# Kernel optimization log

Measured on AMD Instinct MI355X. Metric: run time of the kernel, lower is better.

The kernel has to match this reference:

```python
import jax, jax.numpy as jnp
import numpy as np

B, N, K, NB = 8, 4096, 16, 8
MAX_RADIUS = 10.0
OUT_MUL = 64  # irreps_out = '64x1o' -> output dim 64*3 = 192


def setup_inputs() -> dict:
    key = jax.random.key(0)
    k1, k2 = jax.random.split(key)
    coords = jax.random.normal(k1, (B, N, 3), dtype=jnp.float32)
    tp_weight = jax.random.normal(k2, (1, NB, OUT_MUL), dtype=jnp.float32)
    return {"coords": coords, "tp_weight": tp_weight}


def _knn_indices(coords, k):
    # coords: [B, N, 3] -> nbr idx [B, N, k] (no self loops), per-batch kNN
    n = coords.shape[1]
    d2 = jnp.sum((coords[:, :, None, :] - coords[:, None, :, :]) ** 2, axis=-1)  # [B,N,N]
    d2 = jnp.where(jnp.eye(n, dtype=bool)[None], jnp.inf, d2)
    _, idx = jax.lax.top_k(-d2, k)  # k nearest
    return idx


def reference(coords, tp_weight):
    nbr = _knn_indices(coords, K)                                # [B,N,K] int32
    nbr_coords = jax.vmap(lambda c, i: c[i])(coords, nbr)        # [B,N,K,3]
    r = nbr_coords - coords[:, :, None, :]                       # sender - receiver
    dist = jnp.linalg.norm(r, axis=-1, keepdims=True)            # [B,N,K,1]
    rhat = r / (dist + 1e-8)                                     # 1x1o input
    cutoff = jnp.clip(dist / MAX_RADIUS, 0.0, 1.0)
    # gaussian soft one-hot over [0,1] with NB centers
    centers = jnp.linspace(0.0, 1.0, NB, dtype=coords.dtype)
    sigma = 1.0 / NB
    g = jnp.exp(-((cutoff - centers) ** 2) / (2.0 * sigma * sigma))  # [B,N,K,NB]
    s = jnp.sum(g, axis=-1, keepdims=True)
    rb = g / jnp.where(s > 0, s, jnp.ones_like(s))               # 8x0e input
    # FullyConnectedTensorProduct 1x1o x NBx0e -> OUT_MULx1o (shared weights)
    # path normalization: 1/sqrt(mul_in1 * mul_in2) = 1/sqrt(NB)
    alpha = 1.0 / np.sqrt(1 * NB)
    W = tp_weight[0]                                             # [NB, OUT_MUL]
    edge_feat = alpha * jnp.einsum('vw,bnkv,bnkm->bnkwm', W, rb, rhat)  # [B,N,K,64,3]
    # exactly k incoming edges per receiver -> scatter_mean == mean over K
    agg = jnp.mean(edge_feat, axis=2).reshape(B, N, OUT_MUL * 3)  # [B,N,192]
    return agg
```

## Files before the change

kernel.cpp:

```cpp
#include <hip/hip_runtime.h>

typedef unsigned int u32;
typedef unsigned long long u64;
typedef float v2f __attribute__((ext_vector_type(2)));

#define NBATCH 8
#define NPTS   4096
#define NQTOT  (NBATCH * NPTS)
#define KNN    16
#define NBASIS 8
#define OUTM   64
#define NSPLIT 8
#define WIN    (NPTS / NSPLIT)
#define QPB    64
#define TKNN   (QPB * NSPLIT)
#define GRP    8
#define BUFCAP 64
#define ROWSTR 81
#define TOFF   64

#define SENT 0x7f800000ffffffffull

__device__ __forceinline__ void ce(u64& x, u64& y) {
  u64 a = x, b = y;
  bool sw = b < a;
  x = sw ? b : a;
  y = sw ? a : b;
}

template <int N>
__device__ __forceinline__ void oems_sort(u64* a) {
#pragma unroll
  for (int p = 1; p < N; p <<= 1) {
#pragma unroll
    for (int k = p; k >= 1; k >>= 1) {
#pragma unroll
      for (int j = k & (p - 1); j + k < N; j += 2 * k) {
#pragma unroll
        for (int i = 0; i < k; ++i) {
          int lo = i + j, hi = i + j + k;
          if (hi < N && (lo / (2 * p)) == (hi / (2 * p)))
            ce(a[lo], a[hi]);
        }
      }
    }
  }
}

__device__ __forceinline__ void merge16(u64 t[16], const u64 a[16]) {
  u64 m[16];
#pragma unroll
  for (int i = 0; i < 16; ++i) {
    u64 x = t[i], y = a[15 - i];
    m[i] = (x < y) ? x : y;
  }
#pragma unroll
  for (int k = 8; k >= 1; k >>= 1) {
#pragma unroll
    for (int i = 0; i < 16; ++i) {
      if ((i & k) == 0) ce(m[i], m[i | k]);
    }
  }
#pragma unroll
  for (int i = 0; i < 16; ++i) t[i] = m[i];
}

__device__ __forceinline__ v2f d2pair(v2f cx, v2f cy, v2f cz, v2f qx, v2f qy,
                                      v2f qz) {
#pragma clang fp contract(off)
  v2f dx = cx - qx;
  v2f dy = cy - qy;
  v2f dz = cz - qz;
  v2f d2 = (dx * dx + dy * dy) + dz * dz;
  return d2;
}

__global__ __launch_bounds__(TKNN) void se3_kernel(
    const float* __restrict__ Xp, const float* __restrict__ Yp,
    const float* __restrict__ Zp, const float4* __restrict__ cpad,
    const float* __restrict__ Wmat, float* __restrict__ out) {
  __shared__ u64 sBuf[QPB * ROWSTR];
  __shared__ u32 sCnt[QPB];
  __shared__ float sThr[QPB];
  __shared__ float sM[QPB * 25];

  const int b = blockIdx.x;
  const int qg = blockIdx.y;
  const int tid = threadIdx.x;
  const int ql = tid & 63;
  const int sp = tid >> 6;
  const int qi = qg * QPB + ql;
  const int base = b * NPTS;

  if (tid < QPB) sCnt[tid] = 0;

  const float qx = Xp[base + qi];
  const float qy = Yp[base + qi];
  const float qz = Zp[base + qi];
  const v2f qxx = {qx, qx}, qyy = {qy, qy}, qzz = {qz, qz};

  const int wbase = __builtin_amdgcn_readfirstlane(sp * WIN);
  const v2f* xs2 = (const v2f*)(Xp + base + wbase);
  const v2f* ys2 = (const v2f*)(Yp + base + wbase);
  const v2f* zs2 = (const v2f*)(Zp + base + wbase);
  const int sj = qi - wbase;

  {
    u64 s16[16];
    float cd[16];
#pragma unroll
    for (int p = 0; p < 8; ++p) {
      v2f d2 = d2pair(xs2[p], ys2[p], zs2[p], qxx, qyy, qzz);
      cd[2 * p + 0] = d2.x;
      cd[2 * p + 1] = d2.y;
    }
#pragma unroll
    for (int i = 0; i < 16; ++i) {
      u64 v = ((u64)__float_as_uint(cd[i]) << 32) | (u32)(wbase + i);
      s16[i] = (i == sj) ? SENT : v;
    }
    oems_sort<16>(s16);

    if (sp >= 1 && sp <= 4) {
#pragma unroll
      for (int e = 0; e < 16; ++e)
        sBuf[ql * ROWSTR + (sp - 1) * 16 + e] = s16[e];
    }
    __syncthreads();
    if (sp == 0) {
      u64 t16[16];
#pragma unroll
      for (int e = 0; e < 16; ++e) t16[e] = s16[e];
#pragma unroll
      for (int s = 0; s < 4; ++s) {
        u64 a[16];
#pragma unroll
        for (int e = 0; e < 16; ++e) a[e] = sBuf[ql * ROWSTR + s * 16 + e];
        merge16(t16, a);
      }
#pragma unroll
      for (int e = 0; e < 16; ++e) sBuf[ql * ROWSTR + TOFF + e] = t16[e];
    }
    __syncthreads();
    if (sp >= 5) {
#pragma unroll
      for (int e = 0; e < 16; ++e)
        sBuf[ql * ROWSTR + (sp - 5) * 16 + e] = s16[e];
    }
    __syncthreads();
    if (sp == 0) {
      u64 t16[16];
#pragma unroll
      for (int e = 0; e < 16; ++e) t16[e] = sBuf[ql * ROWSTR + TOFF + e];
#pragma unroll
      for (int s = 0; s < 3; ++s) {
        u64 a[16];
#pragma unroll
        for (int e = 0; e < 16; ++e) a[e] = sBuf[ql * ROWSTR + s * 16 + e];
        merge16(t16, a);
      }
#pragma unroll
      for (int e = 0; e < 16; ++e) sBuf[ql * ROWSTR + TOFF + e] = t16[e];
      sThr[ql] = __uint_as_float((u32)(t16[15] >> 32));
    }
    __syncthreads();
  }
  float thr = sThr[ql];

  const int selfgrp = (sj >= 0 && sj < WIN) ? (sj >> 3) : -1;
  const u32 selfbit = 1u << (sj & 7);

#pragma unroll
  for (int ph = 0; ph < 5; ++ph) {
    const int cstart = 16 << ph;
    const int cend = 32 << ph;
    for (int g = cstart; g < cend; g += GRP) {
      v2f d2p[4];
#pragma unroll
      for (int p = 0; p < 4; ++p)
        d2p[p] = d2pair(xs2[(g >> 1) + p], ys2[(g >> 1) + p],
                        zs2[(g >> 1) + p], qxx, qyy, qzz);
      u32 want = 0;
#pragma unroll
      for (int i = 0; i < GRP; ++i)
        want |= (d2p[i >> 1][i & 1] <= thr) ? (1u << i) : 0u;
      if ((g >> 3) == selfgrp) want &= ~selfbit;
      if (__any(want)) {
#pragma unroll
        for (int i = 0; i < GRP; ++i) {
          if (want & (1u << i)) {
            u32 slot = atomicAdd(&sCnt[ql], 1u);
            if (slot < BUFCAP)
              sBuf[ql * ROWSTR + slot] =
                  ((u64)__float_as_uint(d2p[i >> 1][i & 1]) << 32) |
                  (u32)(wbase + g + i);
          }
        }
      }
    }
    __syncthreads();
    if (sp == ph + 1) {
      int n = (int)sCnt[ql];
      n = n < BUFCAP ? n : BUFCAP;
      if (__any(n > 0)) {
        u64 t16[16];
#pragma unroll
        for (int e = 0; e < 16; ++e) t16[e] = sBuf[ql * ROWSTR + TOFF + e];
        for (int k = 0; __any(k < n); k += 16) {
          u64 a[16];
#pragma unroll
          for (int e = 0; e < 16; ++e)
            a[e] = (k + e < n) ? sBuf[ql * ROWSTR + k + e] : SENT;
          oems_sort<16>(a);
          merge16(t16, a);
        }
#pragma unroll
        for (int e = 0; e < 16; ++e) sBuf[ql * ROWSTR + TOFF + e] = t16[e];
        sThr[ql] = __uint_as_float((u32)(t16[15] >> 32));
      }
      sCnt[ql] = 0;
    }
    __syncthreads();
    thr = sThr[ql];
  }

  if (sp < 4) {
    const int k = sp;
    u64 pv[4];
#pragma unroll
    for (int e = 0; e < 4; ++e)
      pv[e] = sBuf[ql * ROWSTR + TOFF + k * 4 + e];
    float4 nc[4];
    float dd[4];
#pragma unroll
    for (int e = 0; e < 4; ++e) {
      nc[e] = cpad[base + (int)(u32)pv[e]];
      dd[e] = __uint_as_float((u32)(pv[e] >> 32));
    }
    float M[24];
#pragma unroll
    for (int j = 0; j < 24; ++j) M[j] = 0.f;
#pragma unroll
    for (int e = 0; e < 4; ++e) {
      float rx = nc[e].x - qx;
      float ry = nc[e].y - qy;
      float rz = nc[e].z - qz;
      float dist = sqrtf(dd[e]);
      float inv = 1.0f / (dist + 1e-8f);
      rx *= inv; ry *= inv; rz *= inv;
      float cut = fminf(dist * 0.1f, 1.0f);
      float g[NBASIS], s = 0.f;
#pragma unroll
      for (int v = 0; v < NBASIS; ++v) {
        float t = cut - (float)v * (1.0f / 7.0f);
        g[v] = __expf(-32.0f * t * t);
        s += g[v];
      }
      float rs = 1.0f / s;
#pragma unroll
      for (int v = 0; v < NBASIS; ++v) {
        float rb = g[v] * rs;
        M[v * 3 + 0] = fmaf(rb, rx, M[v * 3 + 0]);
        M[v * 3 + 1] = fmaf(rb, ry, M[v * 3 + 1]);
        M[v * 3 + 2] = fmaf(rb, rz, M[v * 3 + 2]);
      }
    }
    float* fp = (float*)(sBuf + ql * ROWSTR);
#pragma unroll
    for (int c = 0; c < 24; ++c) fp[k * 25 + c] = M[c];
  }
  __syncthreads();

  {
    const float* fp = (const float*)(sBuf + ql * ROWSTR);
#pragma unroll
    for (int j0 = 0; j0 < 3; ++j0) {
      int j = sp * 3 + j0;
      float s = fp[0 * 25 + j] + fp[1 * 25 + j] + fp[2 * 25 + j] +
                fp[3 * 25 + j];
      sM[ql * 25 + j] = s;
    }
  }
  __syncthreads();

  float wreg[NBASIS];
#pragma unroll
  for (int v = 0; v < NBASIS; ++v) wreg[v] = Wmat[v * OUTM + ql];
  const float scale = 0.022097086912079608f;
#pragma unroll
  for (int i = 0; i < 8; ++i) {
    int q = sp * 8 + i;
    const float* mq = sM + q * 25;
    float a0 = 0.f, a1 = 0.f, a2 = 0.f;
#pragma unroll
    for (int v = 0; v < NBASIS; ++v) {
      a0 = fmaf(wreg[v], mq[v * 3 + 0], a0);
      a1 = fmaf(wreg[v], mq[v * 3 + 1], a1);
      a2 = fmaf(wreg[v], mq[v * 3 + 2], a2);
    }
    size_t o = (size_t)(base + qg * QPB + q) * (OUTM * 3) + ql * 3;
    out[o + 0] = a0 * scale;
    out[o + 1] = a1 * scale;
    out[o + 2] = a2 * scale;
  }
}

__global__ void prep_kernel(const float* __restrict__ coords,
                            float* __restrict__ Xp, float* __restrict__ Yp,
                            float* __restrict__ Zp, float4* __restrict__ cpad) {
  int i = blockIdx.x * 256 + threadIdx.x;
  if (i < NQTOT) {
    float x = coords[3 * i + 0];
    float y = coords[3 * i + 1];
    float z = coords[3 * i + 2];
    Xp[i] = x; Yp[i] = y; Zp[i] = z;
    cpad[i] = make_float4(x, y, z, 0.f);
  }
}

extern "C" void kernel_launch(void* const* d_in, const int* in_sizes, int n_in,
                              void* d_out, int out_size, void* d_ws, size_t ws_size,
                              hipStream_t stream) {
  const float* coords = (const float*)d_in[0];
  const float* Wmat = (const float*)d_in[1];
  float* out = (float*)d_out;

  char* w = (char*)d_ws;
  float* Xp = (float*)(w);
  float* Yp = (float*)(w + 131072);
  float* Zp = (float*)(w + 262144);
  float4* cpad = (float4*)(w + 393216);

  prep_kernel<<<dim3((NQTOT + 255) / 256), dim3(256), 0, stream>>>(coords, Xp, Yp, Zp, cpad);
  se3_kernel<<<dim3(NBATCH, NPTS / QPB), dim3(TKNN), 0, stream>>>(Xp, Yp, Zp, cpad, Wmat, out);
}
```

Measured before the change: 180.0 us.

## Screen kNN candidates with expanded-norm dot-product test and exact recheck

Replaces the per-candidate squared-distance computation in the candidate scan with an expanded form, 0.5*|c|^2 - c·q, compared against a per-query adjusted threshold. The half-norms are precomputed in the prep kernel and the scan uses 4-wide FMA chains with a group-level min as an early reject. Exact distances are recomputed only for candidates that pass, so the stored keys and ordering stay identical. This lowers ALU work per candidate, with a small safety margin to absorb rounding differences. The float4 padded coordinate array is dropped and the final stage gathers neighbours from the SoA arrays instead.

```diff
diff --git a/kernel.cpp b/kernel.cpp
--- a/kernel.cpp
+++ b/kernel.cpp
@@ -3,6 +3,7 @@
 typedef unsigned int u32;
 typedef unsigned long long u64;
 typedef float v2f __attribute__((ext_vector_type(2)));
+typedef float v4f __attribute__((ext_vector_type(4)));
 
 #define NBATCH 8
 #define NPTS   4096
@@ -18,6 +19,7 @@
 #define BUFCAP 64
 #define ROWSTR 81
 #define TOFF   64
+#define PMARGIN 2e-3f
 
 #define SENT 0x7f800000ffffffffull
 
@@ -75,9 +77,18 @@
   return d2;
 }
 
+__device__ __forceinline__ float d2s(float cx, float cy, float cz, float qx,
+                                     float qy, float qz) {
+#pragma clang fp contract(off)
+  float dx = cx - qx;
+  float dy = cy - qy;
+  float dz = cz - qz;
+  return (dx * dx + dy * dy) + dz * dz;
+}
+
 __global__ __launch_bounds__(TKNN) void se3_kernel(
     const float* __restrict__ Xp, const float* __restrict__ Yp,
-    const float* __restrict__ Zp, const float4* __restrict__ cpad,
+    const float* __restrict__ Zp, const float* __restrict__ Hp,
     const float* __restrict__ Wmat, float* __restrict__ out) {
   __shared__ u64 sBuf[QPB * ROWSTR];
   __shared__ u32 sCnt[QPB];
@@ -98,11 +109,18 @@
   const float qy = Yp[base + qi];
   const float qz = Zp[base + qi];
   const v2f qxx = {qx, qx}, qyy = {qy, qy}, qzz = {qz, qz};
+  const v4f qx4 = {qx, qx, qx, qx};
+  const v4f qy4 = {qy, qy, qy, qy};
+  const v4f qz4 = {qz, qz, qz, qz};
 
   const int wbase = __builtin_amdgcn_readfirstlane(sp * WIN);
   const v2f* xs2 = (const v2f*)(Xp + base + wbase);
   const v2f* ys2 = (const v2f*)(Yp + base + wbase);
   const v2f* zs2 = (const v2f*)(Zp + base + wbase);
+  const v4f* x4 = (const v4f*)(Xp + base + wbase);
+  const v4f* y4 = (const v4f*)(Yp + base + wbase);
+  const v4f* z4 = (const v4f*)(Zp + base + wbase);
+  const v4f* h4 = (const v4f*)(Hp + base + wbase);
   const int sj = qi - wbase;
 
   {
@@ -167,6 +185,9 @@
   }
   float thr = sThr[ql];
 
+  const float qn = qx * qx + qy * qy + qz * qz;
+  float sthr = 0.5f * (thr + PMARGIN - qn);
+
   const int selfgrp = (sj >= 0 && sj < WIN) ? (sj >> 3) : -1;
   const u32 selfbit = 1u << (sj & 7);
 
@@ -175,25 +196,43 @@
     const int cstart = 16 << ph;
     const int cend = 32 << ph;
     for (int g = cstart; g < cend; g += GRP) {
-      v2f d2p[4];
-#pragma unroll
-      for (int p = 0; p < 4; ++p)
-        d2p[p] = d2pair(xs2[(g >> 1) + p], ys2[(g >> 1) + p],
-                        zs2[(g >> 1) + p], qxx, qyy, qzz);
-      u32 want = 0;
-#pragma unroll
-      for (int i = 0; i < GRP; ++i)
-        want |= (d2p[i >> 1][i & 1] <= thr) ? (1u << i) : 0u;
-      if ((g >> 3) == selfgrp) want &= ~selfbit;
-      if (__any(want)) {
-#pragma unroll
-        for (int i = 0; i < GRP; ++i) {
-          if (want & (1u << i)) {
-            u32 slot = atomicAdd(&sCnt[ql], 1u);
-            if (slot < BUFCAP)
-              sBuf[ql * ROWSTR + slot] =
-                  ((u64)__float_as_uint(d2p[i >> 1][i & 1]) << 32) |
-                  (u32)(wbase + g + i);
+      const int gq = g >> 2;
+      v4f XA = x4[gq], XB = x4[gq + 1];
+      v4f YA = y4[gq], YB = y4[gq + 1];
+      v4f ZA = z4[gq], ZB = z4[gq + 1];
+      v4f HA = h4[gq], HB = h4[gq + 1];
+      v4f sA = __builtin_elementwise_fma(
+          -ZA, qz4,
+          __builtin_elementwise_fma(
+              -YA, qy4, __builtin_elementwise_fma(-XA, qx4, HA)));
+      v4f sB = __builtin_elementwise_fma(
+          -ZB, qz4,
+          __builtin_elementwise_fma(
+              -YB, qy4, __builtin_elementwise_fma(-XB, qx4, HB)));
+      v4f m4 = __builtin_elementwise_min(sA, sB);
+      float m = fminf(fminf(m4.x, m4.y), fminf(m4.z, m4.w));
+      if (__any(m <= sthr)) {
+        u32 want = 0;
+#pragma unroll
+        for (int i = 0; i < 4; ++i)
+          want |= (sA[i] <= sthr) ? (1u << i) : 0u;
+#pragma unroll
+        for (int i = 0; i < 4; ++i)
+          want |= (sB[i] <= sthr) ? (1u << (4 + i)) : 0u;
+        if ((g >> 3) == selfgrp) want &= ~selfbit;
+        if (__any(want)) {
+#pragma unroll
+          for (int i = 0; i < GRP; ++i) {
+            if (want & (1u << i)) {
+              float cx = (i < 4) ? XA[i & 3] : XB[i & 3];
+              float cy = (i < 4) ? YA[i & 3] : YB[i & 3];
+              float cz = (i < 4) ? ZA[i & 3] : ZB[i & 3];
+              float d2 = d2s(cx, cy, cz, qx, qy, qz);
+              u32 slot = atomicAdd(&sCnt[ql], 1u);
+              if (slot < BUFCAP)
+                sBuf[ql * ROWSTR + slot] =
+                    ((u64)__float_as_uint(d2) << 32) | (u32)(wbase + g + i);
+            }
           }
         }
       }
@@ -222,6 +261,7 @@
     }
     __syncthreads();
     thr = sThr[ql];
+    sthr = 0.5f * (thr + PMARGIN - qn);
   }
 
   if (sp < 4) {
@@ -230,11 +270,14 @@
 #pragma unroll
     for (int e = 0; e < 4; ++e)
       pv[e] = sBuf[ql * ROWSTR + TOFF + k * 4 + e];
-    float4 nc[4];
+    float ncx[4], ncy[4], ncz[4];
     float dd[4];
 #pragma unroll
     for (int e = 0; e < 4; ++e) {
-      nc[e] = cpad[base + (int)(u32)pv[e]];
+      int id = base + (int)(u32)pv[e];
+      ncx[e] = Xp[id];
+      ncy[e] = Yp[id];
+      ncz[e] = Zp[id];
       dd[e] = __uint_as_float((u32)(pv[e] >> 32));
     }
     float M[24];
@@ -242,9 +285,9 @@
     for (int j = 0; j < 24; ++j) M[j] = 0.f;
 #pragma unroll
     for (int e = 0; e < 4; ++e) {
-      float rx = nc[e].x - qx;
-      float ry = nc[e].y - qy;
-      float rz = nc[e].z - qz;
+      float rx = ncx[e] - qx;
+      float ry = ncy[e] - qy;
+      float rz = ncz[e] - qz;
       float dist = sqrtf(dd[e]);
       float inv = 1.0f / (dist + 1e-8f);
       rx *= inv; ry *= inv; rz *= inv;
@@ -307,14 +350,14 @@
 
 __global__ void prep_kernel(const float* __restrict__ coords,
                             float* __restrict__ Xp, float* __restrict__ Yp,
-                            float* __restrict__ Zp, float4* __restrict__ cpad) {
+                            float* __restrict__ Zp, float* __restrict__ Hp) {
   int i = blockIdx.x * 256 + threadIdx.x;
   if (i < NQTOT) {
     float x = coords[3 * i + 0];
     float y = coords[3 * i + 1];
     float z = coords[3 * i + 2];
     Xp[i] = x; Yp[i] = y; Zp[i] = z;
-    cpad[i] = make_float4(x, y, z, 0.f);
+    Hp[i] = 0.5f * (x * x + y * y + z * z);
   }
 }
 
@@ -329,8 +372,8 @@
   float* Xp = (float*)(w);
   float* Yp = (float*)(w + 131072);
   float* Zp = (float*)(w + 262144);
-  float4* cpad = (float4*)(w + 393216);
-
-  prep_kernel<<<dim3((NQTOT + 255) / 256), dim3(256), 0, stream>>>(coords, Xp, Yp, Zp, cpad);
-  se3_kernel<<<dim3(NBATCH, NPTS / QPB), dim3(TKNN), 0, stream>>>(Xp, Yp, Zp, cpad, Wmat, out);
-}
+  float* Hp = (float*)(w + 393216);
+
+  prep_kernel<<<dim3((NQTOT + 255) / 256), dim3(256), 0, stream>>>(coords, Xp, Yp, Zp, Hp);
+  se3_kernel<<<dim3(NBATCH, NPTS / QPB), dim3(TKNN), 0, stream>>>(Xp, Yp, Zp, Hp, Wmat, out);
+}
```

Result: slower. 184.2 us (+2.3%).

## Split each query's candidate scan across 16 windows with tree-merged top-k

Applied to the files above, without the earlier changes.

Doubles the number of window splits per query, so each block now has 1024 threads that each scan a 256-point window. The serial merge on split 0 is replaced by a pairwise tree reduction of the sorted 16-element lists through shared memory. The threshold-filter phases drop from 5 to 4, and the output loop is spread over twice as many threads. The aim is more parallelism and a shorter serial merge chain, at the cost of more barriers, larger blocks and higher register pressure under the 1024-thread launch bound.

```diff
diff --git a/kernel.cpp b/kernel.cpp
--- a/kernel.cpp
+++ b/kernel.cpp
@@ -10,7 +10,7 @@
 #define KNN    16
 #define NBASIS 8
 #define OUTM   64
-#define NSPLIT 8
+#define NSPLIT 16
 #define WIN    (NPTS / NSPLIT)
 #define QPB    64
 #define TKNN   (QPB * NSPLIT)
@@ -75,6 +75,18 @@
   return d2;
 }
 
+__device__ __forceinline__ void pub16(u64* row, int seg, const u64 s[16]) {
+#pragma unroll
+  for (int e = 0; e < 16; ++e) row[seg * 16 + e] = s[e];
+}
+
+__device__ __forceinline__ void mrg16(const u64* row, int seg, u64 s[16]) {
+  u64 a[16];
+#pragma unroll
+  for (int e = 0; e < 16; ++e) a[e] = row[seg * 16 + e];
+  merge16(s, a);
+}
+
 __global__ __launch_bounds__(TKNN) void se3_kernel(
     const float* __restrict__ Xp, const float* __restrict__ Yp,
     const float* __restrict__ Zp, const float4* __restrict__ cpad,
@@ -105,6 +117,8 @@
   const v2f* zs2 = (const v2f*)(Zp + base + wbase);
   const int sj = qi - wbase;
 
+  u64* row = sBuf + ql * ROWSTR;
+
   {
     u64 s16[16];
     float cd[16];
@@ -121,47 +135,29 @@
     }
     oems_sort<16>(s16);
 
-    if (sp >= 1 && sp <= 4) {
-#pragma unroll
-      for (int e = 0; e < 16; ++e)
-        sBuf[ql * ROWSTR + (sp - 1) * 16 + e] = s16[e];
-    }
+    if (sp >= 8 && sp < 12) pub16(row, sp - 8, s16);
+    __syncthreads();
+    if (sp < 4) mrg16(row, sp, s16);
+    __syncthreads();
+    if (sp >= 12) pub16(row, sp - 12, s16);
+    __syncthreads();
+    if (sp >= 4 && sp < 8) mrg16(row, sp - 4, s16);
+    __syncthreads();
+    if (sp >= 4 && sp < 8) pub16(row, sp - 4, s16);
+    __syncthreads();
+    if (sp < 4) mrg16(row, sp, s16);
+    __syncthreads();
+    if (sp == 2 || sp == 3) pub16(row, sp - 2, s16);
+    __syncthreads();
+    if (sp < 2) mrg16(row, sp, s16);
+    __syncthreads();
+    if (sp == 1) pub16(row, 0, s16);
     __syncthreads();
     if (sp == 0) {
-      u64 t16[16];
-#pragma unroll
-      for (int e = 0; e < 16; ++e) t16[e] = s16[e];
-#pragma unroll
-      for (int s = 0; s < 4; ++s) {
-        u64 a[16];
-#pragma unroll
-        for (int e = 0; e < 16; ++e) a[e] = sBuf[ql * ROWSTR + s * 16 + e];
-        merge16(t16, a);
-      }
-#pragma unroll
-      for (int e = 0; e < 16; ++e) sBuf[ql * ROWSTR + TOFF + e] = t16[e];
-    }
-    __syncthreads();
-    if (sp >= 5) {
-#pragma unroll
-      for (int e = 0; e < 16; ++e)
-        sBuf[ql * ROWSTR + (sp - 5) * 16 + e] = s16[e];
-    }
-    __syncthreads();
-    if (sp == 0) {
-      u64 t16[16];
-#pragma unroll
-      for (int e = 0; e < 16; ++e) t16[e] = sBuf[ql * ROWSTR + TOFF + e];
-#pragma unroll
-      for (int s = 0; s < 3; ++s) {
-        u64 a[16];
-#pragma unroll
-        for (int e = 0; e < 16; ++e) a[e] = sBuf[ql * ROWSTR + s * 16 + e];
-        merge16(t16, a);
-      }
-#pragma unroll
-      for (int e = 0; e < 16; ++e) sBuf[ql * ROWSTR + TOFF + e] = t16[e];
-      sThr[ql] = __uint_as_float((u32)(t16[15] >> 32));
+      mrg16(row, 0, s16);
+#pragma unroll
+      for (int e = 0; e < 16; ++e) row[TOFF + e] = s16[e];
+      sThr[ql] = __uint_as_float((u32)(s16[15] >> 32));
     }
     __syncthreads();
   }
@@ -171,7 +167,7 @@
   const u32 selfbit = 1u << (sj & 7);
 
 #pragma unroll
-  for (int ph = 0; ph < 5; ++ph) {
+  for (int ph = 0; ph < 4; ++ph) {
     const int cstart = 16 << ph;
     const int cend = 32 << ph;
     for (int g = cstart; g < cend; g += GRP) {
@@ -205,17 +201,17 @@
       if (__any(n > 0)) {
         u64 t16[16];
 #pragma unroll
-        for (int e = 0; e < 16; ++e) t16[e] = sBuf[ql * ROWSTR + TOFF + e];
+        for (int e = 0; e < 16; ++e) t16[e] = row[TOFF + e];
         for (int k = 0; __any(k < n); k += 16) {
           u64 a[16];
 #pragma unroll
           for (int e = 0; e < 16; ++e)
-            a[e] = (k + e < n) ? sBuf[ql * ROWSTR + k + e] : SENT;
+            a[e] = (k + e < n) ? row[k + e] : SENT;
           oems_sort<16>(a);
           merge16(t16, a);
         }
 #pragma unroll
-        for (int e = 0; e < 16; ++e) sBuf[ql * ROWSTR + TOFF + e] = t16[e];
+        for (int e = 0; e < 16; ++e) row[TOFF + e] = t16[e];
         sThr[ql] = __uint_as_float((u32)(t16[15] >> 32));
       }
       sCnt[ql] = 0;
@@ -229,7 +225,7 @@
     u64 pv[4];
 #pragma unroll
     for (int e = 0; e < 4; ++e)
-      pv[e] = sBuf[ql * ROWSTR + TOFF + k * 4 + e];
+      pv[e] = row[TOFF + k * 4 + e];
     float4 nc[4];
     float dd[4];
 #pragma unroll
@@ -265,14 +261,14 @@
         M[v * 3 + 2] = fmaf(rb, rz, M[v * 3 + 2]);
       }
     }
-    float* fp = (float*)(sBuf + ql * ROWSTR);
+    float* fp = (float*)row;
 #pragma unroll
     for (int c = 0; c < 24; ++c) fp[k * 25 + c] = M[c];
   }
   __syncthreads();
 
-  {
-    const float* fp = (const float*)(sBuf + ql * ROWSTR);
+  if (sp < 8) {
+    const float* fp = (const float*)row;
 #pragma unroll
     for (int j0 = 0; j0 < 3; ++j0) {
       int j = sp * 3 + j0;
@@ -288,8 +284,8 @@
   for (int v = 0; v < NBASIS; ++v) wreg[v] = Wmat[v * OUTM + ql];
   const float scale = 0.022097086912079608f;
 #pragma unroll
-  for (int i = 0; i < 8; ++i) {
-    int q = sp * 8 + i;
+  for (int i = 0; i < 4; ++i) {
+    int q = sp * 4 + i;
     const float* mq = sM + q * 25;
     float a0 = 0.f, a1 = 0.f, a2 = 0.f;
 #pragma unroll
```

Measured after the change: 190.4 us. 5.8% more time.

## Buffer kNN candidates as group bitmasks and recompute distances at merge time

Applied to the files above, without the earlier changes.

During the candidate scan, each thread now does one shared atomic per group of 8 points that has any hits and stores a packed (mask, base index) word, replacing one atomic and one 64-bit store per candidate. The merging thread unpacks these bitmasks, gathers neighbour coordinates from global memory and recomputes the distances before sorting and merging. This moves atomic contention and LDS traffic off the hot scan loop, but adds global gathers and serial bit extraction to the merge step. Because the buffer now holds up to 64 groups rather than 64 candidates, overflow is much less likely. The scan loop is also unrolled by two.

```diff
diff --git a/kernel.cpp b/kernel.cpp
--- a/kernel.cpp
+++ b/kernel.cpp
@@ -15,7 +15,7 @@
 #define QPB    64
 #define TKNN   (QPB * NSPLIT)
 #define GRP    8
-#define BUFCAP 64
+#define ECAP   64
 #define ROWSTR 81
 #define TOFF   64
 
@@ -75,6 +75,15 @@
   return d2;
 }
 
+__device__ __forceinline__ float d2s(float cx, float cy, float cz, float qx,
+                                     float qy, float qz) {
+#pragma clang fp contract(off)
+  float dx = cx - qx;
+  float dy = cy - qy;
+  float dz = cz - qz;
+  return (dx * dx + dy * dy) + dz * dz;
+}
+
 __global__ __launch_bounds__(TKNN) void se3_kernel(
     const float* __restrict__ Xp, const float* __restrict__ Yp,
     const float* __restrict__ Zp, const float4* __restrict__ cpad,
@@ -105,6 +114,8 @@
   const v2f* zs2 = (const v2f*)(Zp + base + wbase);
   const int sj = qi - wbase;
 
+  u64* row = sBuf + (size_t)ql * ROWSTR;
+
   {
     u64 s16[16];
     float cd[16];
@@ -123,8 +134,7 @@
 
     if (sp >= 1 && sp <= 4) {
 #pragma unroll
-      for (int e = 0; e < 16; ++e)
-        sBuf[ql * ROWSTR + (sp - 1) * 16 + e] = s16[e];
+      for (int e = 0; e < 16; ++e) row[(sp - 1) * 16 + e] = s16[e];
     }
     __syncthreads();
     if (sp == 0) {
@@ -135,32 +145,31 @@
       for (int s = 0; s < 4; ++s) {
         u64 a[16];
 #pragma unroll
-        for (int e = 0; e < 16; ++e) a[e] = sBuf[ql * ROWSTR + s * 16 + e];
+        for (int e = 0; e < 16; ++e) a[e] = row[s * 16 + e];
         merge16(t16, a);
       }
 #pragma unroll
-      for (int e = 0; e < 16; ++e) sBuf[ql * ROWSTR + TOFF + e] = t16[e];
+      for (int e = 0; e < 16; ++e) row[TOFF + e] = t16[e];
     }
     __syncthreads();
     if (sp >= 5) {
 #pragma unroll
-      for (int e = 0; e < 16; ++e)
-        sBuf[ql * ROWSTR + (sp - 5) * 16 + e] = s16[e];
+      for (int e = 0; e < 16; ++e) row[(sp - 5) * 16 + e] = s16[e];
     }
     __syncthreads();
     if (sp == 0) {
       u64 t16[16];
 #pragma unroll
-      for (int e = 0; e < 16; ++e) t16[e] = sBuf[ql * ROWSTR + TOFF + e];
+      for (int e = 0; e < 16; ++e) t16[e] = row[TOFF + e];
 #pragma unroll
       for (int s = 0; s < 3; ++s) {
         u64 a[16];
 #pragma unroll
-        for (int e = 0; e < 16; ++e) a[e] = sBuf[ql * ROWSTR + s * 16 + e];
+        for (int e = 0; e < 16; ++e) a[e] = row[s * 16 + e];
         merge16(t16, a);
       }
 #pragma unroll
-      for (int e = 0; e < 16; ++e) sBuf[ql * ROWSTR + TOFF + e] = t16[e];
+      for (int e = 0; e < 16; ++e) row[TOFF + e] = t16[e];
       sThr[ql] = __uint_as_float((u32)(t16[15] >> 32));
     }
     __syncthreads();
@@ -169,11 +178,14 @@
 
   const int selfgrp = (sj >= 0 && sj < WIN) ? (sj >> 3) : -1;
   const u32 selfbit = 1u << (sj & 7);
+
+  u32* ebuf = (u32*)row;
 
 #pragma unroll
   for (int ph = 0; ph < 5; ++ph) {
     const int cstart = 16 << ph;
     const int cend = 32 << ph;
+#pragma unroll 2
     for (int g = cstart; g < cend; g += GRP) {
       v2f d2p[4];
 #pragma unroll
@@ -185,37 +197,53 @@
       for (int i = 0; i < GRP; ++i)
         want |= (d2p[i >> 1][i & 1] <= thr) ? (1u << i) : 0u;
       if ((g >> 3) == selfgrp) want &= ~selfbit;
-      if (__any(want)) {
-#pragma unroll
-        for (int i = 0; i < GRP; ++i) {
-          if (want & (1u << i)) {
-            u32 slot = atomicAdd(&sCnt[ql], 1u);
-            if (slot < BUFCAP)
-              sBuf[ql * ROWSTR + slot] =
-                  ((u64)__float_as_uint(d2p[i >> 1][i & 1]) << 32) |
-                  (u32)(wbase + g + i);
-          }
-        }
+      if (want) {
+        u32 slot = atomicAdd(&sCnt[ql], 1u);
+        if (slot < ECAP) ebuf[slot] = (want << 12) | (u32)(wbase + g);
       }
     }
     __syncthreads();
     if (sp == ph + 1) {
       int n = (int)sCnt[ql];
-      n = n < BUFCAP ? n : BUFCAP;
+      n = n < ECAP ? n : ECAP;
       if (__any(n > 0)) {
         u64 t16[16];
 #pragma unroll
-        for (int e = 0; e < 16; ++e) t16[e] = sBuf[ql * ROWSTR + TOFF + e];
-        for (int k = 0; __any(k < n); k += 16) {
+        for (int e = 0; e < 16; ++e) t16[e] = row[TOFF + e];
+        int cursor = 0;
+        u32 curWant = 0, curBase = 0;
+        while (__any(cursor < n || curWant != 0)) {
+          u32 kidx[16];
+          u32 vmask = 0;
+#pragma unroll
+          for (int e = 0; e < 16; ++e) {
+            if (curWant == 0 && cursor < n) {
+              u32 ent = ebuf[cursor++];
+              curWant = ent >> 12;
+              curBase = ent & 0xFFFu;
+            }
+            if (curWant) {
+              int bit = __ffs(curWant) - 1;
+              curWant &= curWant - 1;
+              kidx[e] = curBase + (u32)bit;
+              vmask |= (1u << e);
+            } else {
+              kidx[e] = 0;
+            }
+          }
           u64 a[16];
 #pragma unroll
-          for (int e = 0; e < 16; ++e)
-            a[e] = (k + e < n) ? sBuf[ql * ROWSTR + k + e] : SENT;
+          for (int e = 0; e < 16; ++e) {
+            float4 c = cpad[base + (int)kidx[e]];
+            float d2 = d2s(c.x, c.y, c.z, qx, qy, qz);
+            u64 key = ((u64)__float_as_uint(d2) << 32) | kidx[e];
+            a[e] = (vmask & (1u << e)) ? key : SENT;
+          }
           oems_sort<16>(a);
           merge16(t16, a);
         }
 #pragma unroll
-        for (int e = 0; e < 16; ++e) sBuf[ql * ROWSTR + TOFF + e] = t16[e];
+        for (int e = 0; e < 16; ++e) row[TOFF + e] = t16[e];
         sThr[ql] = __uint_as_float((u32)(t16[15] >> 32));
       }
       sCnt[ql] = 0;
@@ -228,8 +256,7 @@
     const int k = sp;
     u64 pv[4];
 #pragma unroll
-    for (int e = 0; e < 4; ++e)
-      pv[e] = sBuf[ql * ROWSTR + TOFF + k * 4 + e];
+    for (int e = 0; e < 4; ++e) pv[e] = row[TOFF + k * 4 + e];
     float4 nc[4];
     float dd[4];
 #pragma unroll
@@ -265,14 +292,14 @@
         M[v * 3 + 2] = fmaf(rb, rz, M[v * 3 + 2]);
       }
     }
-    float* fp = (float*)(sBuf + ql * ROWSTR);
+    float* fp = (float*)row;
 #pragma unroll
     for (int c = 0; c < 24; ++c) fp[k * 25 + c] = M[c];
   }
   __syncthreads();
 
   {
-    const float* fp = (const float*)(sBuf + ql * ROWSTR);
+    const float* fp = (const float*)row;
 #pragma unroll
     for (int j0 = 0; j0 < 3; ++j0) {
       int j = sp * 3 + j0;
```

Result: faster. 170.6 us (-5.2%).
